# Kernel optimization log

Hardware: AMD Instinct MI355X
Metric: run time of the kernel (lower is better)

Reference implementation:

```python
import jax, jax.numpy as jnp
import numpy as np
import math

HIDDEN = 1024
N_HEADS = 16
HEAD = HIDDEN // N_HEADS
NEG_INF = -10000.0


def setup_inputs() -> dict:
    key = jax.random.key(0)
    ks = jax.random.split(key, 5)
    B, S = 4, 2048
    x = jax.random.normal(ks[0], (B, S, HIDDEN), dtype=jnp.float32)
    sc = 1.0 / math.sqrt(HIDDEN)
    qkv_w = jax.random.normal(ks[1], (HIDDEN, 3 * HIDDEN), dtype=jnp.float32) * sc
    qkv_b = jnp.zeros((3 * HIDDEN,), dtype=jnp.float32)
    out_w = jax.random.normal(ks[2], (HIDDEN, HIDDEN), dtype=jnp.float32) * sc
    out_b = jnp.zeros((HIDDEN,), dtype=jnp.float32)
    return {"x": x, "qkv_w": qkv_w, "qkv_b": qkv_b, "out_w": out_w, "out_b": out_b}


def reference(x, qkv_w, qkv_b, out_w, out_b):
    B, S, H = x.shape
    qkv = x @ qkv_w + qkv_b                      # [B,S,3H]
    q, k, v = jnp.split(qkv, 3, axis=-1)
    # b n (h l) -> b h n l
    def heads(t):
        return t.reshape(B, S, N_HEADS, HEAD).transpose(0, 2, 1, 3)
    q, k, v = heads(q), heads(k), heads(v)
    scores = jnp.einsum('bhql,bhkl->bhqk', q, k) / math.sqrt(HEAD)
    q_ind = jnp.arange(S)[:, None]
    k_ind = jnp.arange(S)[None, :]
    mask = q_ind < k_ind                          # future positions
    scores = jnp.where(mask, NEG_INF, scores)
    attn = jax.nn.softmax(scores, axis=-1)
    ctx = jnp.einsum('bhqk,bhkl->bhql', attn, v)  # [B,H,S,l]
    ctx = ctx.transpose(0, 2, 1, 3).reshape(B, S, H)
    return ctx @ out_w + out_b
```

## Files before the change

### kernel.cpp

```cpp
#include <hip/hip_runtime.h>

#define HIDDEN 1024
#define NHEADS 16
#define HEAD   64
#define BATCH  4
#define SEQ    2048
#define BS     (BATCH*SEQ)
#define H3     (3*HIDDEN)

typedef unsigned short u16;
typedef unsigned int   u32;
typedef __bf16 bf16x8 __attribute__((ext_vector_type(8)));
typedef float  f32x4  __attribute__((ext_vector_type(4)));

__device__ __forceinline__ u16 f2bf(float f) {
    union { float f; u32 u; } v; v.f = f;
    u32 u = v.u;
    u32 r = u + 0x7FFFu + ((u >> 16) & 1u);
    return (u16)(r >> 16);
}

__device__ __forceinline__ void gload_lds16(const u16* g, u16* l) {
    __builtin_amdgcn_global_load_lds(
        (const __attribute__((address_space(1))) void*)g,
        (__attribute__((address_space(3))) void*)l, 16, 0, 0);
}

__global__ __launch_bounds__(256) void conv_x(
    const float* __restrict__ in, u16* __restrict__ out)
{
    const size_t i = ((size_t)blockIdx.x * 256 + threadIdx.x) * 8;
    float4 v0 = *(const float4*)&in[i];
    float4 v1 = *(const float4*)&in[i + 4];
    u16 u[8];
    u[0]=f2bf(v0.x); u[1]=f2bf(v0.y); u[2]=f2bf(v0.z); u[3]=f2bf(v0.w);
    u[4]=f2bf(v1.x); u[5]=f2bf(v1.y); u[6]=f2bf(v1.z); u[7]=f2bf(v1.w);
    *(uint4*)&out[i] = *(uint4*)u;
}

__global__ __launch_bounds__(256) void conv_wt(
    const float* __restrict__ w, u16* __restrict__ wt, int N)
{
    __shared__ float tile[64][65];
    const int t  = threadIdx.x;
    const int n0 = blockIdx.x * 64;
    const int k0 = blockIdx.y * 64;
#pragma unroll
    for (int i = 0; i < 4; i++) {
        int kr = i * 16 + (t >> 4);
        int c4 = (t & 15) * 4;
        float4 v = *(const float4*)&w[(size_t)(k0 + kr) * N + n0 + c4];
        tile[kr][c4+0] = v.x; tile[kr][c4+1] = v.y;
        tile[kr][c4+2] = v.z; tile[kr][c4+3] = v.w;
    }
    __syncthreads();
#pragma unroll
    for (int i = 0; i < 4; i++) {
        int nr = i * 16 + (t >> 4);
        int k4 = (t & 15) * 4;
        ushort4 uu;
        uu.x = f2bf(tile[k4+0][nr]); uu.y = f2bf(tile[k4+1][nr]);
        uu.z = f2bf(tile[k4+2][nr]); uu.w = f2bf(tile[k4+3][nr]);
        *(ushort4*)&wt[(size_t)(n0 + nr) * 1024 + k0 + k4] = uu;
    }
}

__global__ __launch_bounds__(256) void qkv_gemm(
    const u16* __restrict__ A, const u16* __restrict__ Bt,
    const float* __restrict__ bias,
    u16* __restrict__ q_ws, u16* __restrict__ k_ws, u16* __restrict__ vt_ws)
{
    __shared__ u16 a_lds[128 * 64];
    __shared__ u16 b_lds[128 * 64];

    const int swz    = (blockIdx.x & 7) * 192 + (blockIdx.x >> 3);
    const int m0     = (swz / 24) * 128;
    const int n0     = (swz % 24) * 128;

    const int t    = threadIdx.x;
    const int lane = t & 63, wv = t >> 6;
    const int lr   = lane & 15, lg = lane >> 4;
    const int wr   = wv >> 1, wc = wv & 1;
    const int srow = wv * 32 + (lane >> 3);
    const int sseg = (lane & 7) * 8;

    f32x4 acc[4][4];
#pragma unroll
    for (int m = 0; m < 4; m++)
#pragma unroll
        for (int n = 0; n < 4; n++)
#pragma unroll
            for (int r = 0; r < 4; r++) acc[m][n][r] = 0.f;

    for (int kt = 0; kt < 16; kt++) {
        const int kk = kt * 64;
        __syncthreads();
#pragma unroll
        for (int i = 0; i < 4; i++) {
            int row = srow + i * 8;
            gload_lds16(&A [(size_t)(m0 + row) * 1024 + kk + sseg], &a_lds[row * 64 + sseg]);
            gload_lds16(&Bt[(size_t)(n0 + row) * 1024 + kk + sseg], &b_lds[row * 64 + sseg]);
        }
        __syncthreads();

        bf16x8 af[2][4], bf[2][4];
#pragma unroll
        for (int ks = 0; ks < 2; ks++) {
#pragma unroll
            for (int m = 0; m < 4; m++)
                af[ks][m] = *(const bf16x8*)&a_lds[(wr * 64 + m * 16 + lr) * 64 + ks * 32 + lg * 8];
#pragma unroll
            for (int n = 0; n < 4; n++)
                bf[ks][n] = *(const bf16x8*)&b_lds[(wc * 64 + n * 16 + lr) * 64 + ks * 32 + lg * 8];
        }
#pragma unroll
        for (int ks = 0; ks < 2; ks++)
#pragma unroll
            for (int m = 0; m < 4; m++)
#pragma unroll
                for (int n = 0; n < 4; n++)
                    acc[m][n] = __builtin_amdgcn_mfma_f32_16x16x32_bf16(af[ks][m], bf[ks][n], acc[m][n], 0, 0, 0);
    }

#pragma unroll
    for (int m = 0; m < 4; m++) {
#pragma unroll
        for (int n = 0; n < 4; n++) {
#pragma unroll
            for (int r = 0; r < 4; r++) {
                int row = m0 + wr * 64 + m * 16 + lg * 4 + r;
                int col = n0 + wc * 64 + n * 16 + lr;
                float val = acc[m][n][r] + bias[col];
                int which = col >> 10;
                int cid   = col & 1023;
                int h = cid >> 6, d = cid & 63;
                int b = row >> 11, s = row & 2047;
                int bh = b * NHEADS + h;
                if (which == 0)
                    q_ws[((size_t)bh * SEQ + s) * HEAD + d] = f2bf(val * 0.125f);
                else if (which == 1)
                    k_ws[((size_t)bh * SEQ + s) * HEAD + d] = f2bf(val);
                else
                    vt_ws[((size_t)bh * HEAD + d) * SEQ + s] = f2bf(val);
            }
        }
    }
}

__global__ __launch_bounds__(256) void out_gemm(
    const u16* __restrict__ A, const u16* __restrict__ Bt,
    const float* __restrict__ bias, float* __restrict__ out)
{
    __shared__ u16 a_lds[128 * 64];
    __shared__ u16 b_lds[128 * 64];

    const int swz = (blockIdx.x & 7) * 64 + (blockIdx.x >> 3);
    const int m0  = (swz >> 3) * 128;
    const int n0  = (swz & 7) * 128;

    const int t    = threadIdx.x;
    const int lane = t & 63, wv = t >> 6;
    const int lr   = lane & 15, lg = lane >> 4;
    const int wr   = wv >> 1, wc = wv & 1;
    const int srow = wv * 32 + (lane >> 3);
    const int sseg = (lane & 7) * 8;

    f32x4 acc[4][4];
#pragma unroll
    for (int m = 0; m < 4; m++)
#pragma unroll
        for (int n = 0; n < 4; n++)
#pragma unroll
            for (int r = 0; r < 4; r++) acc[m][n][r] = 0.f;

    for (int kt = 0; kt < 16; kt++) {
        const int kk = kt * 64;
        __syncthreads();
#pragma unroll
        for (int i = 0; i < 4; i++) {
            int row = srow + i * 8;
            gload_lds16(&A [(size_t)(m0 + row) * 1024 + kk + sseg], &a_lds[row * 64 + sseg]);
            gload_lds16(&Bt[(size_t)(n0 + row) * 1024 + kk + sseg], &b_lds[row * 64 + sseg]);
        }
        __syncthreads();

        bf16x8 af[2][4], bf[2][4];
#pragma unroll
        for (int ks = 0; ks < 2; ks++) {
#pragma unroll
            for (int m = 0; m < 4; m++)
                af[ks][m] = *(const bf16x8*)&a_lds[(wr * 64 + m * 16 + lr) * 64 + ks * 32 + lg * 8];
#pragma unroll
            for (int n = 0; n < 4; n++)
                bf[ks][n] = *(const bf16x8*)&b_lds[(wc * 64 + n * 16 + lr) * 64 + ks * 32 + lg * 8];
        }
#pragma unroll
        for (int ks = 0; ks < 2; ks++)
#pragma unroll
            for (int m = 0; m < 4; m++)
#pragma unroll
                for (int n = 0; n < 4; n++)
                    acc[m][n] = __builtin_amdgcn_mfma_f32_16x16x32_bf16(af[ks][m], bf[ks][n], acc[m][n], 0, 0, 0);
    }

#pragma unroll
    for (int m = 0; m < 4; m++) {
#pragma unroll
        for (int n = 0; n < 4; n++) {
#pragma unroll
            for (int r = 0; r < 4; r++) {
                int row = m0 + wr * 64 + m * 16 + lg * 4 + r;
                int col = n0 + wc * 64 + n * 16 + lr;
                out[(size_t)row * HIDDEN + col] = acc[m][n][r] + bias[col];
            }
        }
    }
}

__global__ __launch_bounds__(256) void attn_kernel(
    const u16* __restrict__ q_ws, const u16* __restrict__ k_ws,
    const u16* __restrict__ vt_ws, u16* __restrict__ ctx_ws)
{
    __shared__ u16 k_lds[2][64][72];
    __shared__ u16 vt_lds[2][64][72];
    __shared__ u16 p_lds[4][16][72];

    const int t  = threadIdx.x;
    const int g  = blockIdx.x;
    const int bh = ((g >> 8) << 3) | (g & 7);
    const int qt = 31 - ((g >> 3) & 31);

    const int lane = t & 63, wv = t >> 6;
    const int lr   = lane & 15, lg = lane >> 4;
    const int srow = t >> 2;
    const int sseg = (t & 3) * 16;

    const u16* kbase = k_ws  + (size_t)bh * SEQ * HEAD;
    const u16* vbase = vt_ws + (size_t)bh * HEAD * SEQ;

    const int qr0 = qt * 64 + wv * 16;
    bf16x8 qa[2];
#pragma unroll
    for (int ks = 0; ks < 2; ks++)
        qa[ks] = *(const bf16x8*)&q_ws[((size_t)bh * SEQ + qr0 + lr) * HEAD + ks * 32 + lg * 8];

    {
        const u16* kp = &kbase[(size_t)srow * HEAD + sseg];
        const u16* vp = &vbase[(size_t)srow * SEQ + sseg];
        uint4 a0 = *(const uint4*)kp;
        uint4 a1 = *(const uint4*)(kp + 8);
        uint4 b0 = *(const uint4*)vp;
        uint4 b1 = *(const uint4*)(vp + 8);
        *(uint4*)&k_lds[0][srow][sseg]      = a0;
        *(uint4*)&k_lds[0][srow][sseg + 8]  = a1;
        *(uint4*)&vt_lds[0][srow][sseg]     = b0;
        *(uint4*)&vt_lds[0][srow][sseg + 8] = b1;
    }
    __syncthreads();

    f32x4 acc_o[4];
#pragma unroll
    for (int df = 0; df < 4; df++)
#pragma unroll
        for (int r = 0; r < 4; r++) acc_o[df][r] = 0.f;
    float m_run[4], l_run[4];
#pragma unroll
    for (int r = 0; r < 4; r++) { m_run[r] = -3e38f; l_run[r] = 0.f; }

    int cur = 0;
    for (int kt = 0; kt <= qt; kt++) {
        const bool pf = (kt < qt);
        uint4 kn0, kn1, vn0, vn1;
        if (pf) {
            const u16* kp = &kbase[(size_t)((kt + 1) * 64 + srow) * HEAD + sseg];
            const u16* vp = &vbase[(size_t)srow * SEQ + (kt + 1) * 64 + sseg];
            kn0 = *(const uint4*)kp;
            kn1 = *(const uint4*)(kp + 8);
            vn0 = *(const uint4*)vp;
            vn1 = *(const uint4*)(vp + 8);
        }

        f32x4 s_acc[4];
#pragma unroll
        for (int nf = 0; nf < 4; nf++) {
#pragma unroll
            for (int r = 0; r < 4; r++) s_acc[nf][r] = 0.f;
#pragma unroll
            for (int ks = 0; ks < 2; ks++) {
                bf16x8 kb = *(const bf16x8*)&k_lds[cur][nf * 16 + lr][ks * 32 + lg * 8];
                s_acc[nf] = __builtin_amdgcn_mfma_f32_16x16x32_bf16(qa[ks], kb, s_acc[nf], 0, 0, 0);
            }
        }

        if (kt == qt) {
#pragma unroll
            for (int nf = 0; nf < 4; nf++)
#pragma unroll
                for (int r = 0; r < 4; r++) {
                    int gq = wv * 16 + lg * 4 + r;
                    int gk = nf * 16 + lr;
                    if (gk > gq) s_acc[nf][r] = -1e9f;
                }
        }

        float p[4][4];
#pragma unroll
        for (int r = 0; r < 4; r++) {
            float mx = fmaxf(fmaxf(s_acc[0][r], s_acc[1][r]), fmaxf(s_acc[2][r], s_acc[3][r]));
#pragma unroll
            for (int off = 8; off >= 1; off >>= 1)
                mx = fmaxf(mx, __shfl_xor(mx, off));
            float m_new = fmaxf(m_run[r], mx);
            float sc = __expf(m_run[r] - m_new);
            float rs = 0.f;
#pragma unroll
            for (int nf = 0; nf < 4; nf++) {
                p[nf][r] = __expf(s_acc[nf][r] - m_new);
                rs += p[nf][r];
            }
#pragma unroll
            for (int off = 8; off >= 1; off >>= 1)
                rs += __shfl_xor(rs, off);
            l_run[r] = l_run[r] * sc + rs;
            m_run[r] = m_new;
#pragma unroll
            for (int df = 0; df < 4; df++) acc_o[df][r] *= sc;
        }

#pragma unroll
        for (int nf = 0; nf < 4; nf++)
#pragma unroll
            for (int r = 0; r < 4; r++)
                p_lds[wv][lg * 4 + r][nf * 16 + lr] = f2bf(p[nf][r]);

        bf16x8 pa[2];
#pragma unroll
        for (int ks = 0; ks < 2; ks++)
            pa[ks] = *(const bf16x8*)&p_lds[wv][lr][ks * 32 + lg * 8];

#pragma unroll
        for (int df = 0; df < 4; df++) {
#pragma unroll
            for (int ks = 0; ks < 2; ks++) {
                bf16x8 vb = *(const bf16x8*)&vt_lds[cur][df * 16 + lr][ks * 32 + lg * 8];
                acc_o[df] = __builtin_amdgcn_mfma_f32_16x16x32_bf16(pa[ks], vb, acc_o[df], 0, 0, 0);
            }
        }

        if (pf) {
            const int nxt = cur ^ 1;
            *(uint4*)&k_lds[nxt][srow][sseg]      = kn0;
            *(uint4*)&k_lds[nxt][srow][sseg + 8]  = kn1;
            *(uint4*)&vt_lds[nxt][srow][sseg]     = vn0;
            *(uint4*)&vt_lds[nxt][srow][sseg + 8] = vn1;
            __syncthreads();
            cur = nxt;
        }
    }

    const int b = bh >> 4, h = bh & 15;
#pragma unroll
    for (int r = 0; r < 4; r++) {
        float inv = 1.f / l_run[r];
        int s = qt * 64 + wv * 16 + lg * 4 + r;
#pragma unroll
        for (int df = 0; df < 4; df++) {
            int d = df * 16 + lr;
            ctx_ws[((size_t)(b * SEQ + s)) * HIDDEN + h * HEAD + d] = f2bf(acc_o[df][r] * inv);
        }
    }
}

extern "C" void kernel_launch(void* const* d_in, const int* in_sizes, int n_in,
                              void* d_out, int out_size, void* d_ws, size_t ws_size,
                              hipStream_t stream)
{
    const float* x    = (const float*)d_in[0];
    const float* qkvw = (const float*)d_in[1];
    const float* qkvb = (const float*)d_in[2];
    const float* outw = (const float*)d_in[3];
    const float* outb = (const float*)d_in[4];
    float* out = (float*)d_out;

    const size_t per = (size_t)BATCH * NHEADS * SEQ * HEAD;
    u16* q_ws   = (u16*)d_ws;
    u16* k_ws   = q_ws + per;
    u16* vt_ws  = k_ws + per;
    u16* c_ws   = vt_ws + per;
    u16* xb     = c_ws + per;
    u16* wqkvt  = xb + per;
    u16* wot    = wqkvt + (size_t)H3 * HIDDEN;

    conv_x <<<dim3((BS * HIDDEN) / (256 * 8)), 256, 0, stream>>>(x, xb);
    conv_wt<<<dim3(H3 / 64, HIDDEN / 64), 256, 0, stream>>>(qkvw, wqkvt, H3);
    conv_wt<<<dim3(HIDDEN / 64, HIDDEN / 64), 256, 0, stream>>>(outw, wot, HIDDEN);

    qkv_gemm<<<dim3(64 * 24), 256, 0, stream>>>(xb, wqkvt, qkvb, q_ws, k_ws, vt_ws);
    attn_kernel<<<dim3(BATCH * NHEADS * (SEQ / 64)), 256, 0, stream>>>(q_ws, k_ws, vt_ws, c_ws);
    out_gemm<<<dim3(64 * 8), 256, 0, stream>>>(c_ws, wot, outb, out);
}
```

Baseline: 373.5 us.

## Use 128-row query tiles with 8 waves sharing K/V tiles in attention

The attention kernel now processes 128 query rows per block with 512 threads (8 waves), so each K/V tile loaded into shared memory is reused by twice as many query rows and the grid is halved. Waves whose rows lie entirely before a key tile skip its compute but still join the barriers. The per-iteration row-sum shuffle reduction is deferred to a single reduction at the end, and bf16 conversion uses the native cast. This trades the lower K/V load traffic for larger blocks, lower occupancy, and idle waves on the diagonal tiles.

```diff
diff --git a/kernel.cpp b/kernel.cpp
--- a/kernel.cpp
+++ b/kernel.cpp
@@ -18,6 +18,12 @@
     u32 u = v.u;
     u32 r = u + 0x7FFFu + ((u >> 16) & 1u);
     return (u16)(r >> 16);
+}
+
+__device__ __forceinline__ u16 f2bf_n(float f) {
+    __bf16 h = (__bf16)f;
+    union { __bf16 h; u16 u; } v; v.h = h;
+    return v.u;
 }
 
 __device__ __forceinline__ void gload_lds16(const u16* g, u16* l) {
@@ -217,44 +223,38 @@
     }
 }
 
-__global__ __launch_bounds__(256) void attn_kernel(
+__global__ __launch_bounds__(512) void attn_kernel(
     const u16* __restrict__ q_ws, const u16* __restrict__ k_ws,
     const u16* __restrict__ vt_ws, u16* __restrict__ ctx_ws)
 {
     __shared__ u16 k_lds[2][64][72];
     __shared__ u16 vt_lds[2][64][72];
-    __shared__ u16 p_lds[4][16][72];
+    __shared__ u16 p_lds[8][16][72];
 
     const int t  = threadIdx.x;
     const int g  = blockIdx.x;
-    const int bh = ((g >> 8) << 3) | (g & 7);
-    const int qt = 31 - ((g >> 3) & 31);
+    const int bh  = ((g >> 7) << 3) | (g & 7);
+    const int qt2 = 15 - ((g >> 3) & 15);
 
     const int lane = t & 63, wv = t >> 6;
     const int lr   = lane & 15, lg = lane >> 4;
-    const int srow = t >> 2;
-    const int sseg = (t & 3) * 16;
+    const int srow = t >> 3;
+    const int sseg = (t & 7) * 8;
 
     const u16* kbase = k_ws  + (size_t)bh * SEQ * HEAD;
     const u16* vbase = vt_ws + (size_t)bh * HEAD * SEQ;
 
-    const int qr0 = qt * 64 + wv * 16;
+    const int qr0 = qt2 * 128 + wv * 16;
     bf16x8 qa[2];
 #pragma unroll
     for (int ks = 0; ks < 2; ks++)
         qa[ks] = *(const bf16x8*)&q_ws[((size_t)bh * SEQ + qr0 + lr) * HEAD + ks * 32 + lg * 8];
 
     {
-        const u16* kp = &kbase[(size_t)srow * HEAD + sseg];
-        const u16* vp = &vbase[(size_t)srow * SEQ + sseg];
-        uint4 a0 = *(const uint4*)kp;
-        uint4 a1 = *(const uint4*)(kp + 8);
-        uint4 b0 = *(const uint4*)vp;
-        uint4 b1 = *(const uint4*)(vp + 8);
-        *(uint4*)&k_lds[0][srow][sseg]      = a0;
-        *(uint4*)&k_lds[0][srow][sseg + 8]  = a1;
-        *(uint4*)&vt_lds[0][srow][sseg]     = b0;
-        *(uint4*)&vt_lds[0][srow][sseg + 8] = b1;
+        uint4 a0 = *(const uint4*)&kbase[(size_t)srow * HEAD + sseg];
+        uint4 b0 = *(const uint4*)&vbase[(size_t)srow * SEQ + sseg];
+        *(uint4*)&k_lds[0][srow][sseg]  = a0;
+        *(uint4*)&vt_lds[0][srow][sseg] = b0;
     }
     __syncthreads();
 
@@ -263,110 +263,113 @@
     for (int df = 0; df < 4; df++)
 #pragma unroll
         for (int r = 0; r < 4; r++) acc_o[df][r] = 0.f;
-    float m_run[4], l_run[4];
-#pragma unroll
-    for (int r = 0; r < 4; r++) { m_run[r] = -3e38f; l_run[r] = 0.f; }
+    float m_run[4], l_part[4];
+#pragma unroll
+    for (int r = 0; r < 4; r++) { m_run[r] = -3e38f; l_part[r] = 0.f; }
 
     int cur = 0;
-    for (int kt = 0; kt <= qt; kt++) {
-        const bool pf = (kt < qt);
-        uint4 kn0, kn1, vn0, vn1;
+    const int ktmax = 2 * qt2 + 1;
+    for (int kt = 0; kt <= ktmax; kt++) {
+        const bool pf = (kt < ktmax);
+        uint4 kn, vn;
         if (pf) {
-            const u16* kp = &kbase[(size_t)((kt + 1) * 64 + srow) * HEAD + sseg];
-            const u16* vp = &vbase[(size_t)srow * SEQ + (kt + 1) * 64 + sseg];
-            kn0 = *(const uint4*)kp;
-            kn1 = *(const uint4*)(kp + 8);
-            vn0 = *(const uint4*)vp;
-            vn1 = *(const uint4*)(vp + 8);
-        }
-
-        f32x4 s_acc[4];
-#pragma unroll
-        for (int nf = 0; nf < 4; nf++) {
-#pragma unroll
-            for (int r = 0; r < 4; r++) s_acc[nf][r] = 0.f;
-#pragma unroll
-            for (int ks = 0; ks < 2; ks++) {
-                bf16x8 kb = *(const bf16x8*)&k_lds[cur][nf * 16 + lr][ks * 32 + lg * 8];
-                s_acc[nf] = __builtin_amdgcn_mfma_f32_16x16x32_bf16(qa[ks], kb, s_acc[nf], 0, 0, 0);
-            }
-        }
-
-        if (kt == qt) {
+            kn = *(const uint4*)&kbase[(size_t)((kt + 1) * 64 + srow) * HEAD + sseg];
+            vn = *(const uint4*)&vbase[(size_t)srow * SEQ + (kt + 1) * 64 + sseg];
+        }
+
+        if (kt * 64 <= qr0 + 15) {
+            f32x4 s_acc[4];
+#pragma unroll
+            for (int nf = 0; nf < 4; nf++) {
+#pragma unroll
+                for (int r = 0; r < 4; r++) s_acc[nf][r] = 0.f;
+#pragma unroll
+                for (int ks = 0; ks < 2; ks++) {
+                    bf16x8 kb = *(const bf16x8*)&k_lds[cur][nf * 16 + lr][ks * 32 + lg * 8];
+                    s_acc[nf] = __builtin_amdgcn_mfma_f32_16x16x32_bf16(qa[ks], kb, s_acc[nf], 0, 0, 0);
+                }
+            }
+
+            if (kt * 64 + 63 > qr0) {
+#pragma unroll
+                for (int nf = 0; nf < 4; nf++)
+#pragma unroll
+                    for (int r = 0; r < 4; r++) {
+                        int gq = qr0 + lg * 4 + r;
+                        int gk = kt * 64 + nf * 16 + lr;
+                        if (gk > gq) s_acc[nf][r] = -1e9f;
+                    }
+            }
+
+            float p[4][4];
+#pragma unroll
+            for (int r = 0; r < 4; r++) {
+                float mx = fmaxf(fmaxf(s_acc[0][r], s_acc[1][r]), fmaxf(s_acc[2][r], s_acc[3][r]));
+#pragma unroll
+                for (int off = 8; off >= 1; off >>= 1)
+                    mx = fmaxf(mx, __shfl_xor(mx, off));
+                float m_new = fmaxf(m_run[r], mx);
+                float sc = __expf(m_run[r] - m_new);
+                float rs;
+                p[0][r] = __expf(s_acc[0][r] - m_new);
+                p[1][r] = __expf(s_acc[1][r] - m_new);
+                p[2][r] = __expf(s_acc[2][r] - m_new);
+                p[3][r] = __expf(s_acc[3][r] - m_new);
+                rs = (p[0][r] + p[1][r]) + (p[2][r] + p[3][r]);
+                l_part[r] = l_part[r] * sc + rs;
+                m_run[r] = m_new;
+#pragma unroll
+                for (int df = 0; df < 4; df++) acc_o[df][r] *= sc;
+            }
+
 #pragma unroll
             for (int nf = 0; nf < 4; nf++)
 #pragma unroll
-                for (int r = 0; r < 4; r++) {
-                    int gq = wv * 16 + lg * 4 + r;
-                    int gk = nf * 16 + lr;
-                    if (gk > gq) s_acc[nf][r] = -1e9f;
+                for (int r = 0; r < 4; r++)
+                    p_lds[wv][lg * 4 + r][nf * 16 + lr] = f2bf_n(p[nf][r]);
+
+            bf16x8 pa[2];
+#pragma unroll
+            for (int ks = 0; ks < 2; ks++)
+                pa[ks] = *(const bf16x8*)&p_lds[wv][lr][ks * 32 + lg * 8];
+
+#pragma unroll
+            for (int df = 0; df < 4; df++) {
+#pragma unroll
+                for (int ks = 0; ks < 2; ks++) {
+                    bf16x8 vb = *(const bf16x8*)&vt_lds[cur][df * 16 + lr][ks * 32 + lg * 8];
+                    acc_o[df] = __builtin_amdgcn_mfma_f32_16x16x32_bf16(pa[ks], vb, acc_o[df], 0, 0, 0);
                 }
-        }
-
-        float p[4][4];
-#pragma unroll
-        for (int r = 0; r < 4; r++) {
-            float mx = fmaxf(fmaxf(s_acc[0][r], s_acc[1][r]), fmaxf(s_acc[2][r], s_acc[3][r]));
-#pragma unroll
-            for (int off = 8; off >= 1; off >>= 1)
-                mx = fmaxf(mx, __shfl_xor(mx, off));
-            float m_new = fmaxf(m_run[r], mx);
-            float sc = __expf(m_run[r] - m_new);
-            float rs = 0.f;
-#pragma unroll
-            for (int nf = 0; nf < 4; nf++) {
-                p[nf][r] = __expf(s_acc[nf][r] - m_new);
-                rs += p[nf][r];
-            }
-#pragma unroll
-            for (int off = 8; off >= 1; off >>= 1)
-                rs += __shfl_xor(rs, off);
-            l_run[r] = l_run[r] * sc + rs;
-            m_run[r] = m_new;
-#pragma unroll
-            for (int df = 0; df < 4; df++) acc_o[df][r] *= sc;
-        }
-
-#pragma unroll
-        for (int nf = 0; nf < 4; nf++)
-#pragma unroll
-            for (int r = 0; r < 4; r++)
-                p_lds[wv][lg * 4 + r][nf * 16 + lr] = f2bf(p[nf][r]);
-
-        bf16x8 pa[2];
-#pragma unroll
-        for (int ks = 0; ks < 2; ks++)
-            pa[ks] = *(const bf16x8*)&p_lds[wv][lr][ks * 32 + lg * 8];
-
-#pragma unroll
-        for (int df = 0; df < 4; df++) {
-#pragma unroll
-            for (int ks = 0; ks < 2; ks++) {
-                bf16x8 vb = *(const bf16x8*)&vt_lds[cur][df * 16 + lr][ks * 32 + lg * 8];
-                acc_o[df] = __builtin_amdgcn_mfma_f32_16x16x32_bf16(pa[ks], vb, acc_o[df], 0, 0, 0);
             }
         }
 
         if (pf) {
             const int nxt = cur ^ 1;
-            *(uint4*)&k_lds[nxt][srow][sseg]      = kn0;
-            *(uint4*)&k_lds[nxt][srow][sseg + 8]  = kn1;
-            *(uint4*)&vt_lds[nxt][srow][sseg]     = vn0;
-            *(uint4*)&vt_lds[nxt][srow][sseg + 8] = vn1;
+            *(uint4*)&k_lds[nxt][srow][sseg]  = kn;
+            *(uint4*)&vt_lds[nxt][srow][sseg] = vn;
             __syncthreads();
             cur = nxt;
         }
     }
 
+    float inv[4];
+#pragma unroll
+    for (int r = 0; r < 4; r++) {
+        float l = l_part[r];
+#pragma unroll
+        for (int off = 8; off >= 1; off >>= 1)
+            l += __shfl_xor(l, off);
+        inv[r] = 1.f / l;
+    }
+
     const int b = bh >> 4, h = bh & 15;
 #pragma unroll
     for (int r = 0; r < 4; r++) {
-        float inv = 1.f / l_run[r];
-        int s = qt * 64 + wv * 16 + lg * 4 + r;
+        int s = qr0 + lg * 4 + r;
 #pragma unroll
         for (int df = 0; df < 4; df++) {
             int d = df * 16 + lr;
-            ctx_ws[((size_t)(b * SEQ + s)) * HIDDEN + h * HEAD + d] = f2bf(acc_o[df][r] * inv);
+            ctx_ws[((size_t)(b * SEQ + s)) * HIDDEN + h * HEAD + d] = f2bf_n(acc_o[df][r] * inv[r]);
         }
     }
 }
@@ -396,6 +399,6 @@
     conv_wt<<<dim3(HIDDEN / 64, HIDDEN / 64), 256, 0, stream>>>(outw, wot, HIDDEN);
 
     qkv_gemm<<<dim3(64 * 24), 256, 0, stream>>>(xb, wqkvt, qkvb, q_ws, k_ws, vt_ws);
-    attn_kernel<<<dim3(BATCH * NHEADS * (SEQ / 64)), 256, 0, stream>>>(q_ws, k_ws, vt_ws, c_ws);
+    attn_kernel<<<dim3(64 * 16), 512, 0, stream>>>(q_ws, k_ws, vt_ws, c_ws);
     out_gemm<<<dim3(64 * 8), 256, 0, stream>>>(c_ws, wot, outb, out);
 }
```

New measurement: 351.0 us. 1.06x faster.
